# Kernel tuning notes

Measured on AMD Instinct MI355X. Metric: run time of the kernel, lower is better.

The kernel has to match this reference:

```python
import jax, jax.numpy as jnp
import numpy as np

B, CIN, COUT, S1, S2, M1, M2 = 16, 64, 64, 128, 128, 16, 16


def _cas(L, dtype):
    # Hartley 'cas' matrix: cos(2*pi*k*k'/L) + sin(2*pi*k*k'/L), symmetric LxL
    k = jnp.arange(L, dtype=dtype)
    ang = (2.0 * jnp.pi / L) * (k[:, None] * k[None, :])
    return jnp.cos(ang) + jnp.sin(ang)


def dht2(x):
    # x: [B, C, M, N] -> dense 2D discrete Hartley transform via matmuls
    M, N = x.shape[-2], x.shape[-1]
    cas_row = _cas(M, x.dtype)
    cas_col = _cas(N, x.dtype)
    # torch: matmul(x, cas_col.T) then matmul(cas_row.T, .)
    y = jnp.einsum('bimn,gn->bimg', x, cas_col)
    return jnp.einsum('mf,bimn->bifn', cas_row, y)


def idht2(x):
    return dht2(x) / (x.shape[-2] * x.shape[-1])


def _neg_freq(a):
    # roll(flip(a, [-1,-2]), (1,1), [-1,-2])
    return jnp.roll(jnp.flip(a, axis=(-2, -1)), shift=(1, 1), axis=(-2, -1))


def compl_mul2d(x1, x2):
    x1n = _neg_freq(x1)
    x2n = _neg_freq(x2)
    e = lambda a, b: jnp.einsum('bixy,ioxy->boxy', a, b)
    return 0.5 * (e(x1, x2) - e(x1n, x2n) + e(x1, x2n) + e(x1n, x2))


def setup_inputs() -> dict:
    key = jax.random.key(0)
    k1, k2, k3 = jax.random.split(key, 3)
    scale = 1.0 / (CIN * COUT)
    x = jax.random.normal(k1, (B, CIN, S1, S2), dtype=jnp.float32)
    weights1 = scale * jax.random.uniform(k2, (CIN, COUT, M1, M2), dtype=jnp.float32)
    weights2 = scale * jax.random.uniform(k3, (CIN, COUT, M1, M2), dtype=jnp.float32)
    return {'x': x, 'weights1': weights1, 'weights2': weights2}


def reference(x, weights1, weights2):
    m1, m2 = weights1.shape[2], weights1.shape[3]
    b, cout = x.shape[0], weights1.shape[1]
    s1, s2 = x.shape[-2], x.shape[-1]

    cos_part = dht2(x)
    sin_part = dht2(jnp.flip(x, axis=(-2, -1)))
    # torch.angle(complex(cos, sin)) == atan2(sin, cos)
    phase = jnp.arctan2(sin_part, cos_part)

    out_dht = jnp.zeros((b, cout, s1, s2), dtype=x.dtype)
    out_dht = out_dht.at[:, :, :m1, :m2].set(
        compl_mul2d(cos_part[:, :, :m1, :m2], weights1))
    out_dht = out_dht.at[:, :, -m1:, :m2].set(
        compl_mul2d(cos_part[:, :, -m1:, :m2], weights2))

    y = idht2(out_dht)
    return y * jnp.cos(phase)
```

## Files before the change

### kernel.cpp

```cpp
#include <hip/hip_runtime.h>

typedef _Float16 f16;
typedef f16 f16x4 __attribute__((ext_vector_type(4)));
typedef f16 f16x8 __attribute__((ext_vector_type(8)));
typedef float f32x4 __attribute__((ext_vector_type(4)));

#define LSCALE 2048.0f
#define LINV   4.8828125e-4f
#define XS 136

#define MFMA(A,B,C) __builtin_amdgcn_mfma_f32_16x16x32_f16(A, B, C, 0, 0, 0)

__device__ __forceinline__ int frag_slot(int row, int k) {
    return ((((row >> 4) * 4 + (k >> 5)) * 64) + ((k >> 3) & 3) * 16 + (row & 15)) * 8 + (k & 7);
}

__global__ void k_cas(float* __restrict__ casf,
                      f16* __restrict__ FAh, f16* __restrict__ FAl,
                      f16* __restrict__ FVh, f16* __restrict__ FVl) {
    int f = blockIdx.x, m = threadIdx.x;
    const float SC = (float)(6.283185307179586 / 128.0);
    float ang = SC * (float)(f * m);
    double a = (double)ang;
    float v = (float)cos(a) + (float)sin(a);
    casf[f * 128 + m] = v;
    f16 h = (f16)v;
    f16 lo = (f16)((v - (float)h) * LSCALE);
    int sA = frag_slot(f, m);
    FAh[sA] = h;
    FAl[sA] = lo;
    int sV = frag_slot(f, 127 - m);
    FVh[sV] = h;
    FVl[sV] = lo;
}

__global__ __launch_bounds__(1024) void k_dht(
    const float* __restrict__ xg,
    const f16* __restrict__ FAh, const f16* __restrict__ FAl,
    const f16* __restrict__ FVh, const f16* __restrict__ FVl,
    float* __restrict__ outbuf,
    float* __restrict__ cp1, float* __restrict__ cp2)
{
    __shared__ __align__(16) char smem[143360];
    f16* Xh  = (f16*)smem;
    f16* Xl  = (f16*)(smem + 35840);
    f16* W1h = (f16*)smem;
    f16* W1l = (f16*)(smem + 35840);
    f16* W2h = (f16*)(smem + 71680);
    f16* W2l = (f16*)(smem + 107520);

    const int img = blockIdx.x;
    const float* X = xg + (size_t)img * 16384;
    const int t = threadIdx.x;
    const int lane = t & 63;
    const int wv = t >> 6;
    const int l15 = lane & 15;
    const int a4 = lane >> 4;

    #pragma unroll
    for (int it = 0; it < 4; ++it) {
        int i = it * 1024 + t;
        int r = i >> 5, c0 = (i & 31) * 4;
        float4 xv = *(const float4*)&X[r * 128 + c0];
        const float* xp = (const float*)&xv;
        f16x4 hv, lv;
        #pragma unroll
        for (int j = 0; j < 4; ++j) {
            f16 h = (f16)xp[j];
            hv[j] = h;
            lv[j] = (f16)((xp[j] - (float)h) * LSCALE);
        }
        *(f16x4*)&Xh[r * XS + c0] = hv;
        *(f16x4*)&Xl[r * XS + c0] = lv;
    }
    __syncthreads();

    const int gw = wv & 7;
    const int mh = (wv >> 3) * 4;
    f32x4 w1hi[4], w1lo[4], w2hi[4], w2lo[4];
    #pragma unroll
    for (int i = 0; i < 4; ++i) {
        w1hi[i] = (f32x4){0.f,0.f,0.f,0.f}; w1lo[i] = (f32x4){0.f,0.f,0.f,0.f};
        w2hi[i] = (f32x4){0.f,0.f,0.f,0.f}; w2lo[i] = (f32x4){0.f,0.f,0.f,0.f};
    }
    {
        #pragma unroll 1
        for (int ks = 0; ks < 4; ++ks) {
            const int toff = ((gw * 4 + ks) * 64 + lane) * 8;
            f16x8 tah = *(const f16x8*)&FAh[toff];
            f16x8 tal = *(const f16x8*)&FAl[toff];
            f16x8 tvh = *(const f16x8*)&FVh[toff];
            f16x8 tvl = *(const f16x8*)&FVl[toff];
            #pragma unroll
            for (int mi = 0; mi < 4; ++mi) {
                const int base = (16 * (mh + mi) + l15) * XS + ks * 32 + 8 * a4;
                f16x8 xh = *(const f16x8*)&Xh[base];
                f16x8 xl = *(const f16x8*)&Xl[base];
                w1hi[mi] = MFMA(tah, xh, w1hi[mi]);
                w1lo[mi] = MFMA(tal, xh, w1lo[mi]);
                w1lo[mi] = MFMA(tah, xl, w1lo[mi]);
                w2hi[mi] = MFMA(tvh, xh, w2hi[mi]);
                w2lo[mi] = MFMA(tvl, xh, w2lo[mi]);
                w2lo[mi] = MFMA(tvh, xl, w2lo[mi]);
            }
        }
    }
    __syncthreads();

    {
        const int g = 16 * gw + 4 * a4;
        #pragma unroll
        for (int mi = 0; mi < 4; ++mi) {
            const int m = 16 * (mh + mi) + l15;
            #pragma unroll
            for (int r = 0; r < 4; ++r) {
                float v1 = w1hi[mi][r] + LINV * w1lo[mi][r];
                f16 h1 = (f16)v1;
                float v2 = w2hi[mi][r] + LINV * w2lo[mi][r];
                f16 h2 = (f16)v2;
                W2h[(g + r) * XS + m] = h2;
                W2l[(g + r) * XS + m] = (f16)((v2 - (float)h2) * LSCALE);
                W1h[(g + r) * XS + m] = h1;
                W1l[(g + r) * XS + m] = (f16)((v1 - (float)h1) * LSCALE);
            }
        }
    }
    __syncthreads();

    const int ft = wv >> 1;
    const int gh = wv & 1;
    f32x4 chi[4], clo[4], shi[4], slo[4];
    #pragma unroll
    for (int i = 0; i < 4; ++i) {
        chi[i] = (f32x4){0.f,0.f,0.f,0.f}; clo[i] = (f32x4){0.f,0.f,0.f,0.f};
        shi[i] = (f32x4){0.f,0.f,0.f,0.f}; slo[i] = (f32x4){0.f,0.f,0.f,0.f};
    }
    {
        #pragma unroll 1
        for (int ks = 0; ks < 4; ++ks) {
            const int toff = ((ft * 4 + ks) * 64 + lane) * 8;
            f16x8 tah = *(const f16x8*)&FAh[toff];
            f16x8 tal = *(const f16x8*)&FAl[toff];
            f16x8 tvh = *(const f16x8*)&FVh[toff];
            f16x8 tvl = *(const f16x8*)&FVl[toff];
            #pragma unroll
            for (int gi = 0; gi < 4; ++gi) {
                const int gt = 4 * gh + gi;
                const int base = (16 * gt + l15) * XS + ks * 32 + 8 * a4;
                f16x8 u1h = *(const f16x8*)&W1h[base];
                f16x8 u1l = *(const f16x8*)&W1l[base];
                f16x8 u2h = *(const f16x8*)&W2h[base];
                f16x8 u2l = *(const f16x8*)&W2l[base];
                chi[gi] = MFMA(tah, u1h, chi[gi]);
                clo[gi] = MFMA(tal, u1h, clo[gi]);
                clo[gi] = MFMA(tah, u1l, clo[gi]);
                shi[gi] = MFMA(tvh, u2h, shi[gi]);
                slo[gi] = MFMA(tvl, u2h, slo[gi]);
                slo[gi] = MFMA(tvh, u2l, slo[gi]);
            }
        }
    }

    f16* cph = (f16*)(outbuf + (size_t)img * 16384);
    #pragma unroll
    for (int gi = 0; gi < 4; ++gi) {
        const int g = 16 * (4 * gh + gi) + l15;
        #pragma unroll
        for (int r = 0; r < 4; ++r) {
            const int f = 16 * ft + 4 * a4 + r;
            float Cv = chi[gi][r] + LINV * clo[gi][r];
            float Sv = shi[gi][r] + LINV * slo[gi][r];
            float d = Cv * Cv + Sv * Sv;
            float cp = (d > 0.f) ? Cv * rsqrtf(d) : 1.0f;
            cph[f * 128 + g] = (f16)cp;
            if (gh == 0 && gi == 0) {
                if (ft == 0)      cp1[img * 256 + f * 16 + l15] = Cv;
                else if (ft == 7) cp2[img * 256 + (f - 112) * 16 + l15] = Cv;
            }
        }
    }
}

__global__ __launch_bounds__(256) void k_inv(
    const float* __restrict__ cp1, const float* __restrict__ cp2,
    const float* __restrict__ w1,  const float* __restrict__ w2,
    const float* __restrict__ cas,
    float* __restrict__ out)
{
    __shared__ float odS[32 * 16];
    __shared__ float casF[128 * 33];
    __shared__ float Rs[128 * 17];
    __shared__ float casG[16 * 128];
    __shared__ __align__(16) unsigned short cphS[16384];

    const int img = blockIdx.x;
    const int b = img >> 6, o = img & 63;
    const int t = threadIdx.x;

    const uint4* cp16 = (const uint4*)(out + (size_t)img * 16384);
    #pragma unroll
    for (int k = 0; k < 8; ++k) {
        int i = k * 256 + t;
        ((uint4*)cphS)[i] = cp16[i];
    }

    {
        const int xx = t >> 4, yy = t & 15;
        const int nx = (16 - xx) & 15, ny = (16 - yy) & 15;
        const int pf = xx * 16 + yy, pn = nx * 16 + ny;
        float acc1 = 0.f, acc2 = 0.f;
        #pragma unroll 4
        for (int i = 0; i < 64; ++i) {
            const int cb = (b * 64 + i) * 256;
            const int wb = (i * 64 + o) * 256;
            float A1  = cp1[cb + pf];
            float A1n = cp1[cb + pn];
            float W1v = w1[wb + pf];
            float W1n = w1[wb + pn];
            acc1 += A1 * (W1v + W1n) + A1n * (W1v - W1n);
            float A2  = cp2[cb + pf];
            float A2n = cp2[cb + pn];
            float W2v = w2[wb + pf];
            float W2n = w2[wb + pn];
            acc2 += A2 * (W2v + W2n) + A2n * (W2v - W2n);
        }
        odS[pf]       = 0.5f * acc1;
        odS[256 + pf] = 0.5f * acc2;
    }

    #pragma unroll
    for (int k = 0; k < 16; ++k) {
        int idx = t + k * 256;
        int s = idx >> 5, j = idx & 31;
        int f = (j < 16) ? j : (96 + j);
        casF[s * 33 + j] = cas[s * 128 + f];
    }
    #pragma unroll
    for (int k = 0; k < 8; ++k) {
        int idx = t + k * 256;
        casG[idx] = cas[idx];
    }
    __syncthreads();

    {
        const int s1 = t >> 1, gb = (t & 1) * 8;
        float acc[8];
        #pragma unroll
        for (int l = 0; l < 8; ++l) acc[l] = 0.f;
        #pragma unroll 4
        for (int j = 0; j < 32; ++j) {
            float cf = casF[s1 * 33 + j];
            #pragma unroll
            for (int l = 0; l < 8; ++l)
                acc[l] = fmaf(cf, odS[j * 16 + gb + l], acc[l]);
        }
        #pragma unroll
        for (int l = 0; l < 8; ++l) Rs[s1 * 17 + gb + l] = acc[l];
    }
    __syncthreads();

    const float inv = 1.0f / 16384.0f;
    const int grp = t >> 5, lane = t & 31;
    const int s2 = lane * 4;
    for (int r = 0; r < 16; ++r) {
        const int s1 = grp * 16 + r;
        float4 acc = {0.f, 0.f, 0.f, 0.f};
        #pragma unroll
        for (int g = 0; g < 16; ++g) {
            float rv = Rs[s1 * 17 + g];
            float4 c4 = *(const float4*)&casG[g * 128 + s2];
            acc.x = fmaf(rv, c4.x, acc.x);
            acc.y = fmaf(rv, c4.y, acc.y);
            acc.z = fmaf(rv, c4.z, acc.z);
            acc.w = fmaf(rv, c4.w, acc.w);
        }
        const f16* ph = (const f16*)cphS + s1 * 128 + s2;
        size_t idx = (size_t)img * 16384 + (size_t)s1 * 128 + s2;
        float4 res;
        res.x = acc.x * inv * (float)ph[0];
        res.y = acc.y * inv * (float)ph[1];
        res.z = acc.z * inv * (float)ph[2];
        res.w = acc.w * inv * (float)ph[3];
        *(float4*)&out[idx] = res;
    }
}

extern "C" void kernel_launch(void* const* d_in, const int* in_sizes, int n_in,
                              void* d_out, int out_size, void* d_ws, size_t ws_size,
                              hipStream_t stream) {
    (void)in_sizes; (void)n_in; (void)out_size; (void)ws_size;
    const float* x  = (const float*)d_in[0];
    const float* w1 = (const float*)d_in[1];
    const float* w2 = (const float*)d_in[2];
    float* out = (float*)d_out;
    float* ws  = (float*)d_ws;

    float* casf = ws;
    f16* FAh = (f16*)(ws + 16384);
    f16* FAl = FAh + 16384;
    f16* FVh = FAl + 16384;
    f16* FVl = FVh + 16384;
    float* cp1 = (float*)(FVl + 16384);
    float* cp2 = cp1 + 262144;

    k_cas<<<dim3(128), dim3(128), 0, stream>>>(casf, FAh, FAl, FVh, FVl);
    k_dht<<<dim3(1024), dim3(1024), 0, stream>>>(x, FAh, FAl, FVh, FVl, out, cp1, cp2);
    k_inv<<<dim3(1024), dim3(256), 0, stream>>>(cp1, cp2, w1, w2, casf, out);
}
```

Before: 139.7 us.

## Retile DHT MFMA stages to 2x2 wave tiles, pad W stride, register-cache phase

Both MFMA stages in the forward DHT kernel move from 1x4 to 2x2 per-wave tiles, so each wave loads two cas fragments and two data fragments per k-step instead of one and four. This cuts LDS traffic per MFMA. The intermediate W buffers get a padded stride of 140 to reduce bank conflicts on the transposed scatter, and are read back as two 4-wide loads. In the inverse kernel the f16 phase plane is loaded straight from global memory into registers instead of being staged through a 32KB LDS buffer, which lowers LDS use and may raise occupancy at the cost of more register pressure.

```diff
diff --git a/kernel.cpp b/kernel.cpp
--- a/kernel.cpp
+++ b/kernel.cpp
@@ -7,7 +7,8 @@
 
 #define LSCALE 2048.0f
 #define LINV   4.8828125e-4f
-#define XS 136
+#define XSX 136
+#define XSW 140
 
 #define MFMA(A,B,C) __builtin_amdgcn_mfma_f32_16x16x32_f16(A, B, C, 0, 0, 0)
 
@@ -43,7 +44,7 @@
 {
     __shared__ __align__(16) char smem[143360];
     f16* Xh  = (f16*)smem;
-    f16* Xl  = (f16*)(smem + 35840);
+    f16* Xl  = (f16*)(smem + 34816);
     f16* W1h = (f16*)smem;
     f16* W1l = (f16*)(smem + 35840);
     f16* W2h = (f16*)(smem + 71680);
@@ -70,115 +71,144 @@
             hv[j] = h;
             lv[j] = (f16)((xp[j] - (float)h) * LSCALE);
         }
-        *(f16x4*)&Xh[r * XS + c0] = hv;
-        *(f16x4*)&Xl[r * XS + c0] = lv;
-    }
-    __syncthreads();
-
-    const int gw = wv & 7;
-    const int mh = (wv >> 3) * 4;
-    f32x4 w1hi[4], w1lo[4], w2hi[4], w2lo[4];
-    #pragma unroll
-    for (int i = 0; i < 4; ++i) {
-        w1hi[i] = (f32x4){0.f,0.f,0.f,0.f}; w1lo[i] = (f32x4){0.f,0.f,0.f,0.f};
-        w2hi[i] = (f32x4){0.f,0.f,0.f,0.f}; w2lo[i] = (f32x4){0.f,0.f,0.f,0.f};
-    }
+        *(f16x4*)&Xh[r * XSX + c0] = hv;
+        *(f16x4*)&Xl[r * XSX + c0] = lv;
+    }
+    __syncthreads();
+
+    const int gq = wv >> 2, mq = wv & 3;
+    f32x4 w1hi[2][2], w1lo[2][2], w2hi[2][2], w2lo[2][2];
+    #pragma unroll
+    for (int i = 0; i < 2; ++i)
+        #pragma unroll
+        for (int j = 0; j < 2; ++j) {
+            w1hi[i][j] = (f32x4){0.f,0.f,0.f,0.f}; w1lo[i][j] = (f32x4){0.f,0.f,0.f,0.f};
+            w2hi[i][j] = (f32x4){0.f,0.f,0.f,0.f}; w2lo[i][j] = (f32x4){0.f,0.f,0.f,0.f};
+        }
     {
         #pragma unroll 1
         for (int ks = 0; ks < 4; ++ks) {
-            const int toff = ((gw * 4 + ks) * 64 + lane) * 8;
-            f16x8 tah = *(const f16x8*)&FAh[toff];
-            f16x8 tal = *(const f16x8*)&FAl[toff];
-            f16x8 tvh = *(const f16x8*)&FVh[toff];
-            f16x8 tvl = *(const f16x8*)&FVl[toff];
-            #pragma unroll
-            for (int mi = 0; mi < 4; ++mi) {
-                const int base = (16 * (mh + mi) + l15) * XS + ks * 32 + 8 * a4;
+            f16x8 tah[2], tal[2], tvh[2], tvl[2];
+            #pragma unroll
+            for (int gt = 0; gt < 2; ++gt) {
+                const int toff = (((2 * gq + gt) * 4 + ks) * 64 + lane) * 8;
+                tah[gt] = *(const f16x8*)&FAh[toff];
+                tal[gt] = *(const f16x8*)&FAl[toff];
+                tvh[gt] = *(const f16x8*)&FVh[toff];
+                tvl[gt] = *(const f16x8*)&FVl[toff];
+            }
+            #pragma unroll
+            for (int mt = 0; mt < 2; ++mt) {
+                const int base = (32 * mq + 16 * mt + l15) * XSX + ks * 32 + 8 * a4;
                 f16x8 xh = *(const f16x8*)&Xh[base];
                 f16x8 xl = *(const f16x8*)&Xl[base];
-                w1hi[mi] = MFMA(tah, xh, w1hi[mi]);
-                w1lo[mi] = MFMA(tal, xh, w1lo[mi]);
-                w1lo[mi] = MFMA(tah, xl, w1lo[mi]);
-                w2hi[mi] = MFMA(tvh, xh, w2hi[mi]);
-                w2lo[mi] = MFMA(tvl, xh, w2lo[mi]);
-                w2lo[mi] = MFMA(tvh, xl, w2lo[mi]);
-            }
-        }
-    }
-    __syncthreads();
-
-    {
-        const int g = 16 * gw + 4 * a4;
-        #pragma unroll
-        for (int mi = 0; mi < 4; ++mi) {
-            const int m = 16 * (mh + mi) + l15;
-            #pragma unroll
-            for (int r = 0; r < 4; ++r) {
-                float v1 = w1hi[mi][r] + LINV * w1lo[mi][r];
-                f16 h1 = (f16)v1;
-                float v2 = w2hi[mi][r] + LINV * w2lo[mi][r];
-                f16 h2 = (f16)v2;
-                W2h[(g + r) * XS + m] = h2;
-                W2l[(g + r) * XS + m] = (f16)((v2 - (float)h2) * LSCALE);
-                W1h[(g + r) * XS + m] = h1;
-                W1l[(g + r) * XS + m] = (f16)((v1 - (float)h1) * LSCALE);
-            }
-        }
-    }
-    __syncthreads();
-
-    const int ft = wv >> 1;
-    const int gh = wv & 1;
-    f32x4 chi[4], clo[4], shi[4], slo[4];
-    #pragma unroll
-    for (int i = 0; i < 4; ++i) {
-        chi[i] = (f32x4){0.f,0.f,0.f,0.f}; clo[i] = (f32x4){0.f,0.f,0.f,0.f};
-        shi[i] = (f32x4){0.f,0.f,0.f,0.f}; slo[i] = (f32x4){0.f,0.f,0.f,0.f};
-    }
+                #pragma unroll
+                for (int gt = 0; gt < 2; ++gt) {
+                    w1hi[gt][mt] = MFMA(tah[gt], xh, w1hi[gt][mt]);
+                    w1lo[gt][mt] = MFMA(tal[gt], xh, w1lo[gt][mt]);
+                    w1lo[gt][mt] = MFMA(tah[gt], xl, w1lo[gt][mt]);
+                    w2hi[gt][mt] = MFMA(tvh[gt], xh, w2hi[gt][mt]);
+                    w2lo[gt][mt] = MFMA(tvl[gt], xh, w2lo[gt][mt]);
+                    w2lo[gt][mt] = MFMA(tvh[gt], xl, w2lo[gt][mt]);
+                }
+            }
+        }
+    }
+    __syncthreads();
+
+    {
+        #pragma unroll
+        for (int gt = 0; gt < 2; ++gt)
+            #pragma unroll
+            for (int mt = 0; mt < 2; ++mt) {
+                const int m = 32 * mq + 16 * mt + l15;
+                #pragma unroll
+                for (int r = 0; r < 4; ++r) {
+                    const int g = 32 * gq + 16 * gt + 4 * a4 + r;
+                    float v1 = w1hi[gt][mt][r] + LINV * w1lo[gt][mt][r];
+                    f16 h1 = (f16)v1;
+                    float v2 = w2hi[gt][mt][r] + LINV * w2lo[gt][mt][r];
+                    f16 h2 = (f16)v2;
+                    W2h[g * XSW + m] = h2;
+                    W2l[g * XSW + m] = (f16)((v2 - (float)h2) * LSCALE);
+                    W1h[g * XSW + m] = h1;
+                    W1l[g * XSW + m] = (f16)((v1 - (float)h1) * LSCALE);
+                }
+            }
+    }
+    __syncthreads();
+
+    const int fq = wv >> 2, gq2 = wv & 3;
+    f32x4 chi[2][2], clo[2][2], shi[2][2], slo[2][2];
+    #pragma unroll
+    for (int i = 0; i < 2; ++i)
+        #pragma unroll
+        for (int j = 0; j < 2; ++j) {
+            chi[i][j] = (f32x4){0.f,0.f,0.f,0.f}; clo[i][j] = (f32x4){0.f,0.f,0.f,0.f};
+            shi[i][j] = (f32x4){0.f,0.f,0.f,0.f}; slo[i][j] = (f32x4){0.f,0.f,0.f,0.f};
+        }
     {
         #pragma unroll 1
         for (int ks = 0; ks < 4; ++ks) {
-            const int toff = ((ft * 4 + ks) * 64 + lane) * 8;
-            f16x8 tah = *(const f16x8*)&FAh[toff];
-            f16x8 tal = *(const f16x8*)&FAl[toff];
-            f16x8 tvh = *(const f16x8*)&FVh[toff];
-            f16x8 tvl = *(const f16x8*)&FVl[toff];
-            #pragma unroll
-            for (int gi = 0; gi < 4; ++gi) {
-                const int gt = 4 * gh + gi;
-                const int base = (16 * gt + l15) * XS + ks * 32 + 8 * a4;
-                f16x8 u1h = *(const f16x8*)&W1h[base];
-                f16x8 u1l = *(const f16x8*)&W1l[base];
-                f16x8 u2h = *(const f16x8*)&W2h[base];
-                f16x8 u2l = *(const f16x8*)&W2l[base];
-                chi[gi] = MFMA(tah, u1h, chi[gi]);
-                clo[gi] = MFMA(tal, u1h, clo[gi]);
-                clo[gi] = MFMA(tah, u1l, clo[gi]);
-                shi[gi] = MFMA(tvh, u2h, shi[gi]);
-                slo[gi] = MFMA(tvl, u2h, slo[gi]);
-                slo[gi] = MFMA(tvh, u2l, slo[gi]);
+            f16x8 tah[2], tal[2], tvh[2], tvl[2];
+            #pragma unroll
+            for (int ft = 0; ft < 2; ++ft) {
+                const int toff = (((2 * fq + ft) * 4 + ks) * 64 + lane) * 8;
+                tah[ft] = *(const f16x8*)&FAh[toff];
+                tal[ft] = *(const f16x8*)&FAl[toff];
+                tvh[ft] = *(const f16x8*)&FVh[toff];
+                tvl[ft] = *(const f16x8*)&FVl[toff];
+            }
+            #pragma unroll
+            for (int gt = 0; gt < 2; ++gt) {
+                const int wb = (32 * gq2 + 16 * gt + l15) * XSW + ks * 32 + 8 * a4;
+                f16x4 a0 = *(const f16x4*)&W1h[wb];
+                f16x4 a1 = *(const f16x4*)&W1h[wb + 4];
+                f16x4 b0 = *(const f16x4*)&W1l[wb];
+                f16x4 b1 = *(const f16x4*)&W1l[wb + 4];
+                f16x4 c0 = *(const f16x4*)&W2h[wb];
+                f16x4 c1 = *(const f16x4*)&W2h[wb + 4];
+                f16x4 d0 = *(const f16x4*)&W2l[wb];
+                f16x4 d1 = *(const f16x4*)&W2l[wb + 4];
+                f16x8 u1h = __builtin_shufflevector(a0, a1, 0,1,2,3,4,5,6,7);
+                f16x8 u1l = __builtin_shufflevector(b0, b1, 0,1,2,3,4,5,6,7);
+                f16x8 u2h = __builtin_shufflevector(c0, c1, 0,1,2,3,4,5,6,7);
+                f16x8 u2l = __builtin_shufflevector(d0, d1, 0,1,2,3,4,5,6,7);
+                #pragma unroll
+                for (int ft = 0; ft < 2; ++ft) {
+                    chi[ft][gt] = MFMA(tah[ft], u1h, chi[ft][gt]);
+                    clo[ft][gt] = MFMA(tal[ft], u1h, clo[ft][gt]);
+                    clo[ft][gt] = MFMA(tah[ft], u1l, clo[ft][gt]);
+                    shi[ft][gt] = MFMA(tvh[ft], u2h, shi[ft][gt]);
+                    slo[ft][gt] = MFMA(tvl[ft], u2h, slo[ft][gt]);
+                    slo[ft][gt] = MFMA(tvh[ft], u2l, slo[ft][gt]);
+                }
             }
         }
     }
 
     f16* cph = (f16*)(outbuf + (size_t)img * 16384);
     #pragma unroll
-    for (int gi = 0; gi < 4; ++gi) {
-        const int g = 16 * (4 * gh + gi) + l15;
-        #pragma unroll
-        for (int r = 0; r < 4; ++r) {
-            const int f = 16 * ft + 4 * a4 + r;
-            float Cv = chi[gi][r] + LINV * clo[gi][r];
-            float Sv = shi[gi][r] + LINV * slo[gi][r];
-            float d = Cv * Cv + Sv * Sv;
-            float cp = (d > 0.f) ? Cv * rsqrtf(d) : 1.0f;
-            cph[f * 128 + g] = (f16)cp;
-            if (gh == 0 && gi == 0) {
-                if (ft == 0)      cp1[img * 256 + f * 16 + l15] = Cv;
-                else if (ft == 7) cp2[img * 256 + (f - 112) * 16 + l15] = Cv;
-            }
-        }
-    }
+    for (int ft = 0; ft < 2; ++ft)
+        #pragma unroll
+        for (int gt = 0; gt < 2; ++gt) {
+            const int g = 32 * gq2 + 16 * gt + l15;
+            #pragma unroll
+            for (int r = 0; r < 4; ++r) {
+                const int f = 32 * fq + 16 * ft + 4 * a4 + r;
+                float Cv = chi[ft][gt][r] + LINV * clo[ft][gt][r];
+                float Sv = shi[ft][gt][r] + LINV * slo[ft][gt][r];
+                float d = Cv * Cv + Sv * Sv;
+                float cp = (d > 0.f) ? Cv * rsqrtf(d) : 1.0f;
+                cph[f * 128 + g] = (f16)cp;
+                if (gq2 == 0 && gt == 0) {
+                    if (fq == 0 && ft == 0)
+                        cp1[img * 256 + f * 16 + g] = Cv;
+                    else if (fq == 3 && ft == 1)
+                        cp2[img * 256 + (f - 112) * 16 + g] = Cv;
+                }
+            }
+        }
 }
 
 __global__ __launch_bounds__(256) void k_inv(
@@ -191,18 +221,10 @@
     __shared__ float casF[128 * 33];
     __shared__ float Rs[128 * 17];
     __shared__ float casG[16 * 128];
-    __shared__ __align__(16) unsigned short cphS[16384];
 
     const int img = blockIdx.x;
     const int b = img >> 6, o = img & 63;
     const int t = threadIdx.x;
-
-    const uint4* cp16 = (const uint4*)(out + (size_t)img * 16384);
-    #pragma unroll
-    for (int k = 0; k < 8; ++k) {
-        int i = k * 256 + t;
-        ((uint4*)cphS)[i] = cp16[i];
-    }
 
     {
         const int xx = t >> 4, yy = t & 15;
@@ -259,9 +281,17 @@
     }
     __syncthreads();
 
-    const float inv = 1.0f / 16384.0f;
     const int grp = t >> 5, lane = t & 31;
     const int s2 = lane * 4;
+    const f16* phg = (const f16*)(out + (size_t)img * 16384);
+    f16x4 phv[16];
+    #pragma unroll
+    for (int r = 0; r < 16; ++r)
+        phv[r] = *(const f16x4*)&phg[(grp * 16 + r) * 128 + s2];
+    __syncthreads();
+
+    const float inv = 1.0f / 16384.0f;
+    #pragma unroll 1
     for (int r = 0; r < 16; ++r) {
         const int s1 = grp * 16 + r;
         float4 acc = {0.f, 0.f, 0.f, 0.f};
@@ -274,13 +304,12 @@
             acc.z = fmaf(rv, c4.z, acc.z);
             acc.w = fmaf(rv, c4.w, acc.w);
         }
-        const f16* ph = (const f16*)cphS + s1 * 128 + s2;
         size_t idx = (size_t)img * 16384 + (size_t)s1 * 128 + s2;
         float4 res;
-        res.x = acc.x * inv * (float)ph[0];
-        res.y = acc.y * inv * (float)ph[1];
-        res.z = acc.z * inv * (float)ph[2];
-        res.w = acc.w * inv * (float)ph[3];
+        res.x = acc.x * inv * (float)phv[r][0];
+        res.y = acc.y * inv * (float)phv[r][1];
+        res.z = acc.z * inv * (float)phv[r][2];
+        res.w = acc.w * inv * (float)phv[r][3];
         *(float4*)&out[idx] = res;
     }
 }
```

New measurement: 228.9 us. 63.9% more time.

## Split forward DHT per image across two blocks to halve LDS footprint

Applied to the files above, without the earlier changes.

The forward DHT kernel now launches two blocks per image, each computing half of the output columns, so the intermediate W buffers only hold 64 rows and shared memory drops from about 140 KB to 70 KB per block. This lets two blocks share a CU, improving occupancy and latency hiding. The cost is that each block redoes the input load and split-precision conversion. The W row stride is padded to 140 to cut LDS bank conflicts, which forces the loads to be split into 4-element reads.

```diff
diff --git a/kernel.cpp b/kernel.cpp
--- a/kernel.cpp
+++ b/kernel.cpp
@@ -7,7 +7,8 @@
 
 #define LSCALE 2048.0f
 #define LINV   4.8828125e-4f
-#define XS 136
+#define XSX 136
+#define XSW 140
 
 #define MFMA(A,B,C) __builtin_amdgcn_mfma_f32_16x16x32_f16(A, B, C, 0, 0, 0)
 
@@ -34,22 +35,23 @@
     FVl[sV] = lo;
 }
 
-__global__ __launch_bounds__(1024) void k_dht(
+__global__ __launch_bounds__(1024, 8) void k_dht(
     const float* __restrict__ xg,
     const f16* __restrict__ FAh, const f16* __restrict__ FAl,
     const f16* __restrict__ FVh, const f16* __restrict__ FVl,
     float* __restrict__ outbuf,
     float* __restrict__ cp1, float* __restrict__ cp2)
 {
-    __shared__ __align__(16) char smem[143360];
+    __shared__ __align__(16) char smem[71680];
     f16* Xh  = (f16*)smem;
-    f16* Xl  = (f16*)(smem + 35840);
+    f16* Xl  = (f16*)(smem + 34816);
     f16* W1h = (f16*)smem;
-    f16* W1l = (f16*)(smem + 35840);
-    f16* W2h = (f16*)(smem + 71680);
-    f16* W2l = (f16*)(smem + 107520);
+    f16* W1l = (f16*)(smem + 17920);
+    f16* W2h = (f16*)(smem + 35840);
+    f16* W2l = (f16*)(smem + 53760);
 
     const int img = blockIdx.x;
+    const int gh  = blockIdx.y;
     const float* X = xg + (size_t)img * 16384;
     const int t = threadIdx.x;
     const int lane = t & 63;
@@ -70,112 +72,120 @@
             hv[j] = h;
             lv[j] = (f16)((xp[j] - (float)h) * LSCALE);
         }
-        *(f16x4*)&Xh[r * XS + c0] = hv;
-        *(f16x4*)&Xl[r * XS + c0] = lv;
-    }
-    __syncthreads();
-
-    const int gw = wv & 7;
-    const int mh = (wv >> 3) * 4;
-    f32x4 w1hi[4], w1lo[4], w2hi[4], w2lo[4];
-    #pragma unroll
-    for (int i = 0; i < 4; ++i) {
+        *(f16x4*)&Xh[r * XSX + c0] = hv;
+        *(f16x4*)&Xl[r * XSX + c0] = lv;
+    }
+    __syncthreads();
+
+    const int gq = wv & 1, mq = wv >> 1;
+    const int Gq = 2 * gh + gq;
+    f32x4 w1hi[2], w1lo[2], w2hi[2], w2lo[2];
+    #pragma unroll
+    for (int i = 0; i < 2; ++i) {
         w1hi[i] = (f32x4){0.f,0.f,0.f,0.f}; w1lo[i] = (f32x4){0.f,0.f,0.f,0.f};
         w2hi[i] = (f32x4){0.f,0.f,0.f,0.f}; w2lo[i] = (f32x4){0.f,0.f,0.f,0.f};
     }
     {
         #pragma unroll 1
         for (int ks = 0; ks < 4; ++ks) {
-            const int toff = ((gw * 4 + ks) * 64 + lane) * 8;
+            const int base = (16 * mq + l15) * XSX + ks * 32 + 8 * a4;
+            f16x8 xh = *(const f16x8*)&Xh[base];
+            f16x8 xl = *(const f16x8*)&Xl[base];
+            #pragma unroll
+            for (int gt = 0; gt < 2; ++gt) {
+                const int toff = (((2 * Gq + gt) * 4 + ks) * 64 + lane) * 8;
+                f16x8 tah = *(const f16x8*)&FAh[toff];
+                f16x8 tal = *(const f16x8*)&FAl[toff];
+                f16x8 tvh = *(const f16x8*)&FVh[toff];
+                f16x8 tvl = *(const f16x8*)&FVl[toff];
+                w1hi[gt] = MFMA(tah, xh, w1hi[gt]);
+                w1lo[gt] = MFMA(tal, xh, w1lo[gt]);
+                w1lo[gt] = MFMA(tah, xl, w1lo[gt]);
+                w2hi[gt] = MFMA(tvh, xh, w2hi[gt]);
+                w2lo[gt] = MFMA(tvl, xh, w2lo[gt]);
+                w2lo[gt] = MFMA(tvh, xl, w2lo[gt]);
+            }
+        }
+    }
+    __syncthreads();
+
+    {
+        const int m = 16 * mq + l15;
+        #pragma unroll
+        for (int gt = 0; gt < 2; ++gt) {
+            #pragma unroll
+            for (int r = 0; r < 4; ++r) {
+                const int g = 32 * gq + 16 * gt + 4 * a4 + r;
+                float v1 = w1hi[gt][r] + LINV * w1lo[gt][r];
+                f16 h1 = (f16)v1;
+                float v2 = w2hi[gt][r] + LINV * w2lo[gt][r];
+                f16 h2 = (f16)v2;
+                W2h[g * XSW + m] = h2;
+                W2l[g * XSW + m] = (f16)((v2 - (float)h2) * LSCALE);
+                W1h[g * XSW + m] = h1;
+                W1l[g * XSW + m] = (f16)((v1 - (float)h1) * LSCALE);
+            }
+        }
+    }
+    __syncthreads();
+
+    const int fq = wv >> 1, gq2 = wv & 1;
+    f32x4 chi[2], clo[2], shi[2], slo[2];
+    #pragma unroll
+    for (int i = 0; i < 2; ++i) {
+        chi[i] = (f32x4){0.f,0.f,0.f,0.f}; clo[i] = (f32x4){0.f,0.f,0.f,0.f};
+        shi[i] = (f32x4){0.f,0.f,0.f,0.f}; slo[i] = (f32x4){0.f,0.f,0.f,0.f};
+    }
+    {
+        #pragma unroll 1
+        for (int ks = 0; ks < 4; ++ks) {
+            const int toff = ((fq * 4 + ks) * 64 + lane) * 8;
             f16x8 tah = *(const f16x8*)&FAh[toff];
             f16x8 tal = *(const f16x8*)&FAl[toff];
             f16x8 tvh = *(const f16x8*)&FVh[toff];
             f16x8 tvl = *(const f16x8*)&FVl[toff];
             #pragma unroll
-            for (int mi = 0; mi < 4; ++mi) {
-                const int base = (16 * (mh + mi) + l15) * XS + ks * 32 + 8 * a4;
-                f16x8 xh = *(const f16x8*)&Xh[base];
-                f16x8 xl = *(const f16x8*)&Xl[base];
-                w1hi[mi] = MFMA(tah, xh, w1hi[mi]);
-                w1lo[mi] = MFMA(tal, xh, w1lo[mi]);
-                w1lo[mi] = MFMA(tah, xl, w1lo[mi]);
-                w2hi[mi] = MFMA(tvh, xh, w2hi[mi]);
-                w2lo[mi] = MFMA(tvl, xh, w2lo[mi]);
-                w2lo[mi] = MFMA(tvh, xl, w2lo[mi]);
+            for (int gt = 0; gt < 2; ++gt) {
+                const int wb = (32 * gq2 + 16 * gt + l15) * XSW + ks * 32 + 8 * a4;
+                f16x4 a0 = *(const f16x4*)&W1h[wb];
+                f16x4 a1 = *(const f16x4*)&W1h[wb + 4];
+                f16x4 b0 = *(const f16x4*)&W1l[wb];
+                f16x4 b1 = *(const f16x4*)&W1l[wb + 4];
+                f16x4 c0 = *(const f16x4*)&W2h[wb];
+                f16x4 c1 = *(const f16x4*)&W2h[wb + 4];
+                f16x4 d0 = *(const f16x4*)&W2l[wb];
+                f16x4 d1 = *(const f16x4*)&W2l[wb + 4];
+                f16x8 u1h = __builtin_shufflevector(a0, a1, 0,1,2,3,4,5,6,7);
+                f16x8 u1l = __builtin_shufflevector(b0, b1, 0,1,2,3,4,5,6,7);
+                f16x8 u2h = __builtin_shufflevector(c0, c1, 0,1,2,3,4,5,6,7);
+                f16x8 u2l = __builtin_shufflevector(d0, d1, 0,1,2,3,4,5,6,7);
+                chi[gt] = MFMA(tah, u1h, chi[gt]);
+                clo[gt] = MFMA(tal, u1h, clo[gt]);
+                clo[gt] = MFMA(tah, u1l, clo[gt]);
+                shi[gt] = MFMA(tvh, u2h, shi[gt]);
+                slo[gt] = MFMA(tvl, u2h, slo[gt]);
+                slo[gt] = MFMA(tvh, u2l, slo[gt]);
             }
         }
     }
-    __syncthreads();
-
-    {
-        const int g = 16 * gw + 4 * a4;
-        #pragma unroll
-        for (int mi = 0; mi < 4; ++mi) {
-            const int m = 16 * (mh + mi) + l15;
-            #pragma unroll
-            for (int r = 0; r < 4; ++r) {
-                float v1 = w1hi[mi][r] + LINV * w1lo[mi][r];
-                f16 h1 = (f16)v1;
-                float v2 = w2hi[mi][r] + LINV * w2lo[mi][r];
-                f16 h2 = (f16)v2;
-                W2h[(g + r) * XS + m] = h2;
-                W2l[(g + r) * XS + m] = (f16)((v2 - (float)h2) * LSCALE);
-                W1h[(g + r) * XS + m] = h1;
-                W1l[(g + r) * XS + m] = (f16)((v1 - (float)h1) * LSCALE);
-            }
-        }
-    }
-    __syncthreads();
-
-    const int ft = wv >> 1;
-    const int gh = wv & 1;
-    f32x4 chi[4], clo[4], shi[4], slo[4];
-    #pragma unroll
-    for (int i = 0; i < 4; ++i) {
-        chi[i] = (f32x4){0.f,0.f,0.f,0.f}; clo[i] = (f32x4){0.f,0.f,0.f,0.f};
-        shi[i] = (f32x4){0.f,0.f,0.f,0.f}; slo[i] = (f32x4){0.f,0.f,0.f,0.f};
-    }
-    {
-        #pragma unroll 1
-        for (int ks = 0; ks < 4; ++ks) {
-            const int toff = ((ft * 4 + ks) * 64 + lane) * 8;
-            f16x8 tah = *(const f16x8*)&FAh[toff];
-            f16x8 tal = *(const f16x8*)&FAl[toff];
-            f16x8 tvh = *(const f16x8*)&FVh[toff];
-            f16x8 tvl = *(const f16x8*)&FVl[toff];
-            #pragma unroll
-            for (int gi = 0; gi < 4; ++gi) {
-                const int gt = 4 * gh + gi;
-                const int base = (16 * gt + l15) * XS + ks * 32 + 8 * a4;
-                f16x8 u1h = *(const f16x8*)&W1h[base];
-                f16x8 u1l = *(const f16x8*)&W1l[base];
-                f16x8 u2h = *(const f16x8*)&W2h[base];
-                f16x8 u2l = *(const f16x8*)&W2l[base];
-                chi[gi] = MFMA(tah, u1h, chi[gi]);
-                clo[gi] = MFMA(tal, u1h, clo[gi]);
-                clo[gi] = MFMA(tah, u1l, clo[gi]);
-                shi[gi] = MFMA(tvh, u2h, shi[gi]);
-                slo[gi] = MFMA(tvl, u2h, slo[gi]);
-                slo[gi] = MFMA(tvh, u2l, slo[gi]);
-            }
-        }
-    }
 
     f16* cph = (f16*)(outbuf + (size_t)img * 16384);
     #pragma unroll
-    for (int gi = 0; gi < 4; ++gi) {
-        const int g = 16 * (4 * gh + gi) + l15;
+    for (int gt = 0; gt < 2; ++gt) {
+        const int g = 64 * gh + 32 * gq2 + 16 * gt + l15;
         #pragma unroll
         for (int r = 0; r < 4; ++r) {
-            const int f = 16 * ft + 4 * a4 + r;
-            float Cv = chi[gi][r] + LINV * clo[gi][r];
-            float Sv = shi[gi][r] + LINV * slo[gi][r];
+            const int f = 16 * fq + 4 * a4 + r;
+            float Cv = chi[gt][r] + LINV * clo[gt][r];
+            float Sv = shi[gt][r] + LINV * slo[gt][r];
             float d = Cv * Cv + Sv * Sv;
             float cp = (d > 0.f) ? Cv * rsqrtf(d) : 1.0f;
             cph[f * 128 + g] = (f16)cp;
-            if (gh == 0 && gi == 0) {
-                if (ft == 0)      cp1[img * 256 + f * 16 + l15] = Cv;
-                else if (ft == 7) cp2[img * 256 + (f - 112) * 16 + l15] = Cv;
+            if (gh == 0 && gq2 == 0 && gt == 0) {
+                if (fq == 0)
+                    cp1[img * 256 + f * 16 + l15] = Cv;
+                else if (fq == 7)
+                    cp2[img * 256 + (f - 112) * 16 + l15] = Cv;
             }
         }
     }
@@ -304,6 +314,6 @@
     float* cp2 = cp1 + 262144;
 
     k_cas<<<dim3(128), dim3(128), 0, stream>>>(casf, FAh, FAl, FVh, FVl);
-    k_dht<<<dim3(1024), dim3(1024), 0, stream>>>(x, FAh, FAl, FVh, FVl, out, cp1, cp2);
+    k_dht<<<dim3(1024, 2), dim3(1024), 0, stream>>>(x, FAh, FAl, FVh, FVl, out, cp1, cp2);
     k_inv<<<dim3(1024), dim3(256), 0, stream>>>(cp1, cp2, w1, w2, casf, out);
 }
```

New measurement: 155.1 us. +11.0%, slower.
